# Kernel optimization log

Hardware: AMD Instinct MI355X
Metric: run time of the kernel (lower is better)

The kernel has to match this reference:

```python
import jax, jax.numpy as jnp
import numpy as np

EPS = 1e-5

def setup_inputs() -> dict:
    key = jax.random.key(0)
    k1, k2 = jax.random.split(key)
    x = jax.random.normal(k1, (32, 256, 56, 56), dtype=jnp.float32)
    conv_w = jax.random.normal(k2, (1, 2, 5, 5), dtype=jnp.float32) * 0.1
    gamma = jnp.ones((1,), dtype=jnp.float32)
    beta = jnp.zeros((1,), dtype=jnp.float32)
    return {"x": x, "conv_w": conv_w, "gamma": gamma, "beta": beta}

def reference(x, conv_w, gamma, beta):
    # channel max and mean -> [N, 2, H, W]
    y = jnp.stack([jnp.max(x, axis=1), jnp.mean(x, axis=1)], axis=1)
    # 5x5 conv, 2->1 channels, SAME padding, no bias -> [N, 1, H, W]
    y = jax.lax.conv_general_dilated(
        y, conv_w, window_strides=(1, 1), padding=((2, 2), (2, 2)),
        dimension_numbers=("NCHW", "OIHW", "NCHW"))
    # BatchNorm2d(1) in training mode: batch statistics over (N, H, W)
    mean = jnp.mean(y, axis=(0, 2, 3), keepdims=True)
    var = jnp.mean(jnp.square(y - mean), axis=(0, 2, 3), keepdims=True)
    y = (y - mean) * jax.lax.rsqrt(var + EPS)
    y = y * gamma.reshape(1, -1, 1, 1) + beta.reshape(1, -1, 1, 1)
    # double sigmoid gate, broadcast over channels
    return x * jax.nn.sigmoid(jax.nn.sigmoid(y))
```

## Files before the change

kernel.cpp:

```cpp
#include <hip/hip_runtime.h>

#define NN 32
#define CC 256
#define HH 56
#define WW 56
#define HWSZ 3136
#define QPP 784
#define NHW 100352
#define TOT4 6422528

__global__ __launch_bounds__(256) void k_pool(const float* __restrict__ x,
                                              float* __restrict__ pool,
                                              float* __restrict__ stats) {
    if (blockIdx.x == 0 && threadIdx.x == 0 && threadIdx.y == 0) {
        stats[0] = 0.f;
        stats[1] = 0.f;
    }
    const int tx = threadIdx.x;
    const int ty = threadIdx.y;
    const int qid = blockIdx.x * 64 + tx;
    const int n = qid / QPP;
    const int hwq = qid - n * QPP;

    const float4* p = (const float4*)x + (size_t)(n * CC + ty * 64) * QPP + hwq;
    float4 v0 = p[0];
    float4 vmax = v0;
    float4 vsum = v0;
#pragma unroll 8
    for (int i = 1; i < 64; ++i) {
        float4 v = p[(size_t)i * QPP];
        vmax.x = fmaxf(vmax.x, v.x); vmax.y = fmaxf(vmax.y, v.y);
        vmax.z = fmaxf(vmax.z, v.z); vmax.w = fmaxf(vmax.w, v.w);
        vsum.x += v.x; vsum.y += v.y; vsum.z += v.z; vsum.w += v.w;
    }
    __shared__ float4 smax[4][64];
    __shared__ float4 ssum[4][64];
    smax[ty][tx] = vmax;
    ssum[ty][tx] = vsum;
    __syncthreads();
    if (ty == 0) {
        float4 m = smax[0][tx];
        float4 s = ssum[0][tx];
#pragma unroll
        for (int g = 1; g < 4; ++g) {
            float4 mg = smax[g][tx];
            float4 sg = ssum[g][tx];
            m.x = fmaxf(m.x, mg.x); m.y = fmaxf(m.y, mg.y);
            m.z = fmaxf(m.z, mg.z); m.w = fmaxf(m.w, mg.w);
            s.x += sg.x; s.y += sg.y; s.z += sg.z; s.w += sg.w;
        }
        float4* pm = (float4*)pool + (size_t)n * 2 * QPP + hwq;
        pm[0] = m;
        float4 mean;
        const float inv = 1.f / 256.f;
        mean.x = s.x * inv; mean.y = s.y * inv;
        mean.z = s.z * inv; mean.w = s.w * inv;
        pm[QPP] = mean;
    }
}

__global__ __launch_bounds__(256) void k_conv(const float* __restrict__ pool,
                                              const float* __restrict__ cw,
                                              float* __restrict__ conv,
                                              float* __restrict__ stats) {
    __shared__ float w[50];
    const int tid = threadIdx.x;
    if (tid < 50) w[tid] = cw[tid];
    __syncthreads();

    const int gid = blockIdx.x * 256 + tid;
    const int n = gid / HWSZ;
    const int hw = gid - n * HWSZ;
    const int h = hw / WW;
    const int wc = hw - h * WW;

    const float* pb = pool + (size_t)n * 2 * HWSZ;
    float acc = 0.f;
#pragma unroll
    for (int ci = 0; ci < 2; ++ci) {
#pragma unroll
        for (int kh = 0; kh < 5; ++kh) {
            const int hh = h + kh - 2;
            if (hh < 0 || hh >= HH) continue;
#pragma unroll
            for (int kw = 0; kw < 5; ++kw) {
                const int wwc = wc + kw - 2;
                if (wwc < 0 || wwc >= WW) continue;
                acc += pb[ci * HWSZ + hh * WW + wwc] * w[ci * 25 + kh * 5 + kw];
            }
        }
    }
    conv[gid] = acc;

    float s = acc;
    float s2 = acc * acc;
#pragma unroll
    for (int i = 1; i < 64; i <<= 1) {
        s += __shfl_xor(s, i);
        s2 += __shfl_xor(s2, i);
    }
    if ((tid & 63) == 0) {
        atomicAdd(&stats[0], s);
        atomicAdd(&stats[1], s2);
    }
}

__global__ __launch_bounds__(256) void k_gate(const float* __restrict__ conv,
                                              const float* __restrict__ stats,
                                              const float* __restrict__ gamma,
                                              const float* __restrict__ beta,
                                              float* __restrict__ gate) {
    const int gid = blockIdx.x * 256 + threadIdx.x;
    const float invM = 1.f / (float)NHW;
    const float mean = stats[0] * invM;
    const float var = stats[1] * invM - mean * mean;
    const float scale = rsqrtf(var + 1e-5f) * gamma[0];
    const float shift = beta[0] - mean * scale;
    const float v = conv[gid] * scale + shift;
    const float s1 = 1.f / (1.f + __expf(-v));
    gate[gid] = 1.f / (1.f + __expf(-s1));
}

__global__ __launch_bounds__(256) void k_apply(const float* __restrict__ x,
                                               const float* __restrict__ gate,
                                               float* __restrict__ out) {
    const float4* x4 = (const float4*)x;
    const float4* g4 = (const float4*)gate;
    float4* o4 = (float4*)out;
    for (int q = blockIdx.x * blockDim.x + threadIdx.x; q < TOT4;
         q += gridDim.x * blockDim.x) {
        const int plane = q / QPP;
        const int hwq = q - plane * QPP;
        const int n = plane >> 8;
        float4 xv = x4[q];
        float4 gv = g4[n * QPP + hwq];
        float4 r;
        r.x = xv.x * gv.x; r.y = xv.y * gv.y;
        r.z = xv.z * gv.z; r.w = xv.w * gv.w;
        o4[q] = r;
    }
}

extern "C" void kernel_launch(void* const* d_in, const int* in_sizes, int n_in,
                              void* d_out, int out_size, void* d_ws, size_t ws_size,
                              hipStream_t stream) {
    const float* x = (const float*)d_in[0];
    const float* cw = (const float*)d_in[1];
    const float* gamma = (const float*)d_in[2];
    const float* beta = (const float*)d_in[3];
    float* out = (float*)d_out;

    float* ws = (float*)d_ws;
    float* pool = ws;
    float* conv = ws + 2 * NHW;
    float* gate = ws + 3 * NHW;
    float* stats = ws + 4 * NHW;

    k_pool<<<392, dim3(64, 4), 0, stream>>>(x, pool, stats);
    k_conv<<<392, 256, 0, stream>>>(pool, cw, conv, stats);
    k_gate<<<392, 256, 0, stream>>>(conv, stats, gamma, beta, gate);
    k_apply<<<2048, 256, 0, stream>>>(x, gate, out);
}
```

Baseline: 100.4 us.

## Fuse gate computation into apply kernel and widen pooling channel split

Removes the separate gate kernel: the apply kernel now reads the conv map, computes the batch-norm scale/shift and the double sigmoid inline, then multiplies x. The pooling kernel uses 8 channel groups of 32 instead of 4 of 64 with 512-thread blocks to expose more memory parallelism, and the apply grid is doubled. This saves one launch and a gate buffer round-trip, in exchange for recomputing the sigmoids once per channel (256x redundant transcendental work per pixel).

Measured after the change: 99.38 us. Within noise of the previous version (-1.0%).

```diff
diff --git a/kernel.cpp b/kernel.cpp
--- a/kernel.cpp
+++ b/kernel.cpp
@@ -9,7 +9,7 @@
 #define NHW 100352
 #define TOT4 6422528
 
-__global__ __launch_bounds__(256) void k_pool(const float* __restrict__ x,
+__global__ __launch_bounds__(512) void k_pool(const float* __restrict__ x,
                                               float* __restrict__ pool,
                                               float* __restrict__ stats) {
     if (blockIdx.x == 0 && threadIdx.x == 0 && threadIdx.y == 0) {
@@ -22,19 +22,19 @@
     const int n = qid / QPP;
     const int hwq = qid - n * QPP;
 
-    const float4* p = (const float4*)x + (size_t)(n * CC + ty * 64) * QPP + hwq;
+    const float4* p = (const float4*)x + (size_t)(n * CC + ty * 32) * QPP + hwq;
     float4 v0 = p[0];
     float4 vmax = v0;
     float4 vsum = v0;
 #pragma unroll 8
-    for (int i = 1; i < 64; ++i) {
+    for (int i = 1; i < 32; ++i) {
         float4 v = p[(size_t)i * QPP];
         vmax.x = fmaxf(vmax.x, v.x); vmax.y = fmaxf(vmax.y, v.y);
         vmax.z = fmaxf(vmax.z, v.z); vmax.w = fmaxf(vmax.w, v.w);
         vsum.x += v.x; vsum.y += v.y; vsum.z += v.z; vsum.w += v.w;
     }
-    __shared__ float4 smax[4][64];
-    __shared__ float4 ssum[4][64];
+    __shared__ float4 smax[8][64];
+    __shared__ float4 ssum[8][64];
     smax[ty][tx] = vmax;
     ssum[ty][tx] = vsum;
     __syncthreads();
@@ -42,7 +42,7 @@
         float4 m = smax[0][tx];
         float4 s = ssum[0][tx];
 #pragma unroll
-        for (int g = 1; g < 4; ++g) {
+        for (int g = 1; g < 8; ++g) {
             float4 mg = smax[g][tx];
             float4 sg = ssum[g][tx];
             m.x = fmaxf(m.x, mg.x); m.y = fmaxf(m.y, mg.y);
@@ -105,38 +105,49 @@
     }
 }
 
-__global__ __launch_bounds__(256) void k_gate(const float* __restrict__ conv,
-                                              const float* __restrict__ stats,
-                                              const float* __restrict__ gamma,
-                                              const float* __restrict__ beta,
-                                              float* __restrict__ gate) {
-    const int gid = blockIdx.x * 256 + threadIdx.x;
+__global__ __launch_bounds__(256) void k_apply(const float* __restrict__ x,
+                                               const float* __restrict__ conv,
+                                               const float* __restrict__ stats,
+                                               const float* __restrict__ gamma,
+                                               const float* __restrict__ beta,
+                                               float* __restrict__ out) {
     const float invM = 1.f / (float)NHW;
     const float mean = stats[0] * invM;
     const float var = stats[1] * invM - mean * mean;
     const float scale = rsqrtf(var + 1e-5f) * gamma[0];
     const float shift = beta[0] - mean * scale;
-    const float v = conv[gid] * scale + shift;
-    const float s1 = 1.f / (1.f + __expf(-v));
-    gate[gid] = 1.f / (1.f + __expf(-s1));
-}
 
-__global__ __launch_bounds__(256) void k_apply(const float* __restrict__ x,
-                                               const float* __restrict__ gate,
-                                               float* __restrict__ out) {
     const float4* x4 = (const float4*)x;
-    const float4* g4 = (const float4*)gate;
+    const float4* c4 = (const float4*)conv;
     float4* o4 = (float4*)out;
     for (int q = blockIdx.x * blockDim.x + threadIdx.x; q < TOT4;
          q += gridDim.x * blockDim.x) {
         const int plane = q / QPP;
         const int hwq = q - plane * QPP;
         const int n = plane >> 8;
+        float4 cv = c4[n * QPP + hwq];
         float4 xv = x4[q];
-        float4 gv = g4[n * QPP + hwq];
         float4 r;
-        r.x = xv.x * gv.x; r.y = xv.y * gv.y;
-        r.z = xv.z * gv.z; r.w = xv.w * gv.w;
+        {
+            float v = cv.x * scale + shift;
+            float s1 = 1.f / (1.f + __expf(-v));
+            r.x = xv.x * (1.f / (1.f + __expf(-s1)));
+        }
+        {
+            float v = cv.y * scale + shift;
+            float s1 = 1.f / (1.f + __expf(-v));
+            r.y = xv.y * (1.f / (1.f + __expf(-s1)));
+        }
+        {
+            float v = cv.z * scale + shift;
+            float s1 = 1.f / (1.f + __expf(-v));
+            r.z = xv.z * (1.f / (1.f + __expf(-s1)));
+        }
+        {
+            float v = cv.w * scale + shift;
+            float s1 = 1.f / (1.f + __expf(-v));
+            r.w = xv.w * (1.f / (1.f + __expf(-s1)));
+        }
         o4[q] = r;
     }
 }
@@ -153,11 +164,9 @@
     float* ws = (float*)d_ws;
     float* pool = ws;
     float* conv = ws + 2 * NHW;
-    float* gate = ws + 3 * NHW;
-    float* stats = ws + 4 * NHW;
+    float* stats = ws + 3 * NHW;
 
-    k_pool<<<392, dim3(64, 4), 0, stream>>>(x, pool, stats);
+    k_pool<<<392, dim3(64, 8), 0, stream>>>(x, pool, stats);
     k_conv<<<392, 256, 0, stream>>>(pool, cw, conv, stats);
-    k_gate<<<392, 256, 0, stream>>>(conv, stats, gamma, beta, gate);
-    k_apply<<<2048, 256, 0, stream>>>(x, gate, out);
+    k_apply<<<4096, 256, 0, stream>>>(x, conv, stats, gamma, beta, out);
 }
```
